# Performance work log

Hardware: AMD Instinct MI355X
Metric: run time of the kernel (lower is better)

Reference implementation:

```python
import jax, jax.numpy as jnp
import numpy as np

B, S, D = 2, 2048, 4096
H, KV, HD = 32, 8, 128          # n_heads, n_kv_heads, head_dim
N_REP = H // KV                  # GQA repeat factor = 4
ROPE_THETA = 500000.0


def _rope_tables(seqlen, head_dim, theta):
    inv_freq = 1.0 / (theta ** (np.arange(0, head_dim, 2, dtype=np.float32) / head_dim))
    angles = np.outer(np.arange(seqlen, dtype=np.float32), inv_freq)  # [S, HD/2]
    return jnp.asarray(np.cos(angles)), jnp.asarray(np.sin(angles))


def setup_inputs() -> dict:
    key = jax.random.key(0)
    ks = jax.random.split(key, 6)
    x = jax.random.normal(ks[0], (B, S, D), dtype=jnp.float32)
    freqs_cos, freqs_sin = _rope_tables(S, HD, ROPE_THETA)
    # causal additive mask, broadcast over (batch, heads)
    mask = jnp.where(jnp.tril(jnp.ones((S, S), dtype=bool)), 0.0, -jnp.inf).astype(jnp.float32)
    sc = 0.02
    wq = sc * jax.random.normal(ks[1], (D, H * HD), dtype=jnp.float32)   # (in, out)
    wk = sc * jax.random.normal(ks[2], (D, KV * HD), dtype=jnp.float32)
    wv = sc * jax.random.normal(ks[3], (D, KV * HD), dtype=jnp.float32)
    wo = sc * jax.random.normal(ks[4], (H * HD, D), dtype=jnp.float32)
    return {"x": x, "freqs_cos": freqs_cos, "freqs_sin": freqs_sin, "mask": mask,
            "wq": wq, "wk": wk, "wv": wv, "wo": wo}


def _apply_rope(t, cos, sin):
    # t: [B, S, nh, HD]; cos/sin: [S, HD/2]. Complex rotation on adjacent pairs.
    t2 = t.reshape(*t.shape[:-1], HD // 2, 2)
    t0, t1 = t2[..., 0], t2[..., 1]
    c = cos[None, :, None, :]
    s = sin[None, :, None, :]
    r0 = t0 * c - t1 * s
    r1 = t0 * s + t1 * c
    return jnp.stack([r0, r1], axis=-1).reshape(t.shape)


def reference(x, freqs_cos, freqs_sin, mask, wq, wk, wv, wo):
    bsz, seqlen, _ = x.shape
    xq = (x @ wq).reshape(bsz, seqlen, H, HD)
    xk = (x @ wk).reshape(bsz, seqlen, KV, HD)
    xv = (x @ wv).reshape(bsz, seqlen, KV, HD)
    xq = _apply_rope(xq, freqs_cos, freqs_sin)
    xk = _apply_rope(xk, freqs_cos, freqs_sin)
    # repeat_kv (GQA) -> [B, S, H, HD]
    keys = jnp.repeat(xk, N_REP, axis=2)
    values = jnp.repeat(xv, N_REP, axis=2)
    scores = jnp.einsum('bqhd,bkhd->bhqk', xq, keys) / jnp.sqrt(jnp.float32(HD))
    scores = scores + mask[None, None, :, :]
    probs = jax.nn.softmax(scores.astype(jnp.float32), axis=-1).astype(xq.dtype)
    out = jnp.einsum('bhqk,bkhd->bqhd', probs, values).reshape(bsz, seqlen, H * HD)
    return out @ wo
```

## Files before the change

kernel.cpp:

```cpp
#include <hip/hip_runtime.h>
#include <stdint.h>

#define B_ 2
#define S_ 2048
#define D_ 4096
#define H_ 32
#define KV_ 8
#define HD_ 128
#define M_ (B_*S_)
#define NQ_ (H_*HD_)
#define NKV_ (KV_*HD_)

typedef unsigned short u16;
typedef __bf16 bf16x8 __attribute__((ext_vector_type(8)));
typedef float f32x4 __attribute__((ext_vector_type(4)));
typedef u16 u16x8 __attribute__((ext_vector_type(8)));
typedef u16 u16x4 __attribute__((ext_vector_type(4)));

__device__ __forceinline__ u16 f2bf(float f) {
  union { float f; unsigned u; } v; v.f = f;
  unsigned r = v.u + 0x7fffu + ((v.u >> 16) & 1u);
  return (u16)(r >> 16);
}
__device__ __forceinline__ u16 f2bft(float f) {
  union { float f; unsigned u; } v; v.f = f;
  return (u16)(v.u >> 16);
}
__device__ __forceinline__ float bf2f(u16 u) {
  union { unsigned u; float f; } v; v.u = ((unsigned)u) << 16;
  return v.f;
}
__device__ __forceinline__ f32x4 mfma16(bf16x8 a, bf16x8 b, f32x4 c) {
  return __builtin_amdgcn_mfma_f32_16x16x32_bf16(a, b, c, 0, 0, 0);
}

#define GLDS16(gp, lp) __builtin_amdgcn_global_load_lds( \
    (const __attribute__((address_space(1))) unsigned int*)(gp), \
    (__attribute__((address_space(3))) unsigned int*)(lp), 16, 0, 0)

__global__ __launch_bounds__(256) void cvt_bf16(const float* __restrict__ in,
                                                u16* __restrict__ out, int n) {
  int i = (blockIdx.x * 256 + threadIdx.x) * 8;
  if (i >= n) return;
  float4 a = *(const float4*)(in + i);
  float4 b = *(const float4*)(in + i + 4);
  u16x8 o;
  o[0]=f2bf(a.x); o[1]=f2bf(a.y); o[2]=f2bf(a.z); o[3]=f2bf(a.w);
  o[4]=f2bf(b.x); o[5]=f2bf(b.y); o[6]=f2bf(b.z); o[7]=f2bf(b.w);
  *(u16x8*)(out + i) = o;
}

__global__ __launch_bounds__(256) void tcvt(const float* __restrict__ in,
                                            u16* __restrict__ out, int R, int C) {
  __shared__ __attribute__((aligned(16))) u16 tile[32][33];
  int c0 = blockIdx.x * 32, r0 = blockIdx.y * 32;
  int tx = threadIdx.x & 31, ty = threadIdx.x >> 5;
  #pragma unroll
  for (int j = ty; j < 32; j += 8)
    tile[j][tx] = f2bf(in[(size_t)(r0 + j) * C + c0 + tx]);
  __syncthreads();
  #pragma unroll
  for (int j = ty; j < 32; j += 8)
    out[(size_t)(c0 + j) * R + r0 + tx] = tile[tx][j];
}

template<int OUTMODE>
__global__ __launch_bounds__(256) void gemm_bt(const u16* __restrict__ A,
    const u16* __restrict__ BT, void* __restrict__ Cv, void* __restrict__ Cv2,
    int M, int N, int K) {
  __shared__ __attribute__((aligned(16))) u16 As[128 * 32];
  __shared__ __attribute__((aligned(16))) u16 Bs[128 * 32];
  const int tid = threadIdx.x;
  const int bn0 = blockIdx.x * 128, bm0 = blockIdx.y * 128;
  const int w = tid >> 6, l = tid & 63, g = l >> 4, q = l & 15;
  const int wm = (w >> 1) * 64, wn = (w & 1) * 64;
  f32x4 acc[4][4] = {};
  for (int kt = 0; kt < K; kt += 32) {
    __syncthreads();
    #pragma unroll
    for (int p = 0; p < 2; ++p) {
      int c = tid + p * 256;
      int row = c >> 2, slot = c & 3;
      int srck = (slot ^ ((row >> 1) & 3)) << 3;
      GLDS16(A + (size_t)(bm0 + row) * K + kt + srck, As + c * 8);
      GLDS16(BT + (size_t)(bn0 + row) * K + kt + srck, Bs + c * 8);
    }
    __syncthreads();
    bf16x8 af[4], bfr[4];
    #pragma unroll
    for (int m = 0; m < 4; ++m) {
      int row = wm + m * 16 + q;
      af[m] = *(const bf16x8*)(As + row * 32 + ((g ^ ((row >> 1) & 3)) << 3));
    }
    #pragma unroll
    for (int n = 0; n < 4; ++n) {
      int row = wn + n * 16 + q;
      bfr[n] = *(const bf16x8*)(Bs + row * 32 + ((g ^ ((row >> 1) & 3)) << 3));
    }
    #pragma unroll
    for (int m = 0; m < 4; ++m)
      #pragma unroll
      for (int n = 0; n < 4; ++n)
        acc[m][n] = mfma16(af[m], bfr[n], acc[m][n]);
  }
  #pragma unroll
  for (int m = 0; m < 4; ++m)
    #pragma unroll
    for (int n = 0; n < 4; ++n) {
      if (OUTMODE == 3) {
        int row0 = bm0 + wm + m * 16 + g * 4;
        int col  = bn0 + wn + n * 16 + q;
        if (col < 1024) {
          #pragma unroll
          for (int j = 0; j < 4; ++j)
            ((u16*)Cv)[(size_t)(row0 + j) * 1024 + col] = f2bf(acc[m][n][j]);
        } else {
          int c2 = col - 1024;
          u16x4 pk;
          #pragma unroll
          for (int j = 0; j < 4; ++j) pk[j] = f2bf(acc[m][n][j]);
          size_t off = ((size_t)((row0 >> 11) * KV_ + (c2 >> 7)) * 32 + ((row0 >> 6) & 31)) * 8192
                     + (size_t)(c2 & 127) * 64 + (row0 & 63);
          *(u16x4*)((u16*)Cv2 + off) = pk;
        }
      } else {
        #pragma unroll
        for (int j = 0; j < 4; ++j) {
          size_t off = (size_t)(bm0 + wm + m * 16 + g * 4 + j) * N + (bn0 + wn + n * 16 + q);
          if (OUTMODE == 1) ((float*)Cv)[off] = acc[m][n][j];
          else              ((u16*)Cv)[off]  = f2bf(acc[m][n][j]);
        }
      }
    }
}

template<int OUTMODE>
__global__ __launch_bounds__(512, 2) void gemm256(const u16* __restrict__ A,
    const u16* __restrict__ BT, void* __restrict__ Cv, int M, int N, int K) {
  extern __shared__ __attribute__((aligned(16))) u16 DL[];
  const int tid = threadIdx.x;
  const int bn0 = blockIdx.x * 256, bm0 = blockIdx.y * 256;
  const int l = tid & 63, g = l >> 4, q = l & 15;
  const int w = tid >> 6;
  const int wm = (w >> 2) * 128, wn = (w & 3) * 64;
  const int nt = K >> 6;
  f32x4 acc[8][4] = {};

  auto STAGE = [&](int t, int buf) {
    const int kt = t << 6;
    u16* Ad = DL + buf * 32768;
    u16* Bd = Ad + 16384;
    #pragma unroll
    for (int p = 0; p < 4; ++p) {
      int idx = tid + p * 512;
      int row = idx >> 3, slot = idx & 7;
      int sk = (slot ^ (row & 7)) << 3;
      GLDS16(A + (size_t)(bm0 + row) * K + kt + sk, Ad + idx * 8);
    }
    #pragma unroll
    for (int p = 0; p < 4; ++p) {
      int idx = tid + p * 512;
      int row = idx >> 3, slot = idx & 7;
      int sk = (slot ^ (row & 7)) << 3;
      GLDS16(BT + (size_t)(bn0 + row) * K + kt + sk, Bd + idx * 8);
    }
  };

  STAGE(0, 0);
  STAGE(1, 1);
  asm volatile("s_waitcnt vmcnt(8)" ::: "memory");
  __builtin_amdgcn_s_barrier();

  for (int t = 0; t < nt; ++t) {
    const int buf = t & 1;
    const u16* As = DL + buf * 32768;
    const u16* Bs = As + 16384;
    #pragma unroll
    for (int ks = 0; ks < 2; ++ks) {
      bf16x8 a[8], bb[2];
      #pragma unroll
      for (int m = 0; m < 8; ++m) {
        int row = wm + m * 16 + q;
        a[m] = *(const bf16x8*)(As + row * 64 + (((ks * 4 + g) ^ (row & 7)) << 3));
      }
      #pragma unroll
      for (int n = 0; n < 2; ++n) {
        int row = wn + n * 16 + q;
        bb[n] = *(const bf16x8*)(Bs + row * 64 + (((ks * 4 + g) ^ (row & 7)) << 3));
      }
      __builtin_amdgcn_s_setprio(1);
      #pragma unroll
      for (int m = 0; m < 8; ++m)
        #pragma unroll
        for (int n = 0; n < 2; ++n)
          acc[m][n] = mfma16(a[m], bb[n], acc[m][n]);
      __builtin_amdgcn_s_setprio(0);
      #pragma unroll
      for (int n = 0; n < 2; ++n) {
        int row = wn + (n + 2) * 16 + q;
        bb[n] = *(const bf16x8*)(Bs + row * 64 + (((ks * 4 + g) ^ (row & 7)) << 3));
      }
      __builtin_amdgcn_s_setprio(1);
      #pragma unroll
      for (int m = 0; m < 8; ++m)
        #pragma unroll
        for (int n = 0; n < 2; ++n)
          acc[m][n + 2] = mfma16(a[m], bb[n], acc[m][n + 2]);
      __builtin_amdgcn_s_setprio(0);
    }
    if (t + 1 < nt) {
      asm volatile("s_waitcnt lgkmcnt(0)" ::: "memory");
      __builtin_amdgcn_s_barrier();
      if (t + 2 < nt) {
        STAGE(t + 2, buf);
        asm volatile("s_waitcnt vmcnt(8)" ::: "memory");
      } else {
        asm volatile("s_waitcnt vmcnt(0)" ::: "memory");
      }
      __builtin_amdgcn_s_barrier();
    }
  }

  #pragma unroll
  for (int m = 0; m < 8; ++m)
    #pragma unroll
    for (int n = 0; n < 4; ++n)
      #pragma unroll
      for (int j = 0; j < 4; ++j) {
        size_t off = (size_t)(bm0 + wm + m * 16 + g * 4 + j) * N + (bn0 + wn + n * 16 + q);
        if (OUTMODE == 1) ((float*)Cv)[off] = acc[m][n][j];
        else              ((u16*)Cv)[off]  = f2bf(acc[m][n][j]);
      }
}

__global__ __launch_bounds__(256) void rope_kernel(u16* __restrict__ t,
    const float* __restrict__ fc, const float* __restrict__ fs,
    int log2ppr, int total_pairs) {
  int i = blockIdx.x * 256 + threadIdx.x;
  if (i >= total_pairs) return;
  int fi = i & 63;
  int row = i >> log2ppr;
  int pos = row & (S_ - 1);
  float c = fc[pos * 64 + fi], s = fs[pos * 64 + fi];
  unsigned* p = (unsigned*)(t + 2 * (size_t)i);
  unsigned v = *p;
  float x0 = bf2f((u16)(v & 0xffffu)), x1 = bf2f((u16)(v >> 16));
  float r0 = x0 * c - x1 * s, r1 = x0 * s + x1 * c;
  *p = (unsigned)f2bf(r0) | ((unsigned)f2bf(r1) << 16);
}

__global__ __launch_bounds__(256, 4) void attn_kernel(
    const u16* __restrict__ Qb, const u16* __restrict__ Kb,
    const u16* __restrict__ VTg, u16* __restrict__ Ob) {
  __shared__ __attribute__((aligned(16))) u16 SM[20480];
  u16* Ks = SM;
  u16* Vs = SM + 8192;
  u16* Ps = SM + 16384;
  const int pr = blockIdx.x;
  const int h = blockIdx.y, b = blockIdx.z;
  const int kvh = h >> 2;
  const int tid = threadIdx.x, w = tid >> 6, l = tid & 63, g = l >> 4, ql = l & 15;
  const float SL2E = 0.08838834764831845f * 1.4426950408889634f;
  const u16* Qh = Qb + (size_t)b * S_ * NQ_ + h * HD_;
  const u16* Kh = Kb + ((size_t)b * S_ * KV_ + kvh) * HD_;
  const u16* Vh = VTg + (size_t)(b * KV_ + kvh) * (32 * 8192);
  u16* Oh = Ob + (size_t)b * S_ * NQ_ + h * HD_;

  for (int ph = 0; ph < 2; ++ph) {
    const int qt = ph ? pr : 31 - pr;
    __syncthreads();
    bf16x8 aq[4];
    #pragma unroll
    for (int kk = 0; kk < 4; ++kk)
      aq[kk] = *(const bf16x8*)(Qh + (size_t)(qt * 64 + w * 16 + ql) * NQ_ + kk * 32 + g * 8);

    f32x4 o[8] = {};
    float mrow = -3.0e38f, lrow = 0.f;

    const int nkt = qt + 1;
    for (int kt = 0; kt < nkt; ++kt) {
      #pragma unroll
      for (int p = 0; p < 4; ++p) {
        int c = tid + p * 256;
        int row = c >> 4, slot = c & 15;
        GLDS16(Kh + (size_t)(kt * 64 + row) * (KV_ * HD_) + ((slot ^ (row & 7)) << 3), Ks + c * 8);
      }
      #pragma unroll
      for (int p = 0; p < 4; ++p) {
        int c = tid + p * 256;
        int row = c >> 3, slot = c & 7;
        GLDS16(Vh + (size_t)kt * 8192 + row * 64 + ((slot ^ (row & 7)) << 3), Vs + c * 8);
      }
      asm volatile("s_waitcnt vmcnt(0)" ::: "memory");
      __builtin_amdgcn_s_barrier();

      if (kt * 64 <= qt * 64 + w * 16 + 15) {
        f32x4 sc[4] = {};
        #pragma unroll
        for (int kk = 0; kk < 4; ++kk) {
          bf16x8 bk[4];
          #pragma unroll
          for (int n = 0; n < 4; ++n) {
            int row = n * 16 + ql;
            bk[n] = *(const bf16x8*)(Ks + row * 128 + (((kk * 4 + g) ^ (row & 7)) << 3));
          }
          #pragma unroll
          for (int n = 0; n < 4; ++n)
            sc[n] = mfma16(bk[n], aq[kk], sc[n]);
        }
        const int qglob = qt * 64 + w * 16 + ql;
        if (kt * 64 + 63 > qt * 64 + w * 16) {
          #pragma unroll
          for (int n = 0; n < 4; ++n)
            #pragma unroll
            for (int j = 0; j < 4; ++j)
              if (kt * 64 + n * 16 + g * 4 + j > qglob) sc[n][j] = -3.0e38f;
        }
        float mx = sc[0][0];
        #pragma unroll
        for (int n = 0; n < 4; ++n)
          #pragma unroll
          for (int j = 0; j < 4; ++j) mx = fmaxf(mx, sc[n][j]);
        mx = fmaxf(mx, __shfl_xor(mx, 16));
        mx = fmaxf(mx, __shfl_xor(mx, 32));
        if (!__all(mx - mrow <= 16.0f)) {
          float mnew = fmaxf(mrow, mx);
          float f = exp2f((mrow - mnew) * SL2E);
          lrow *= f;
          #pragma unroll
          for (int m = 0; m < 8; ++m) o[m] *= f;
          mrow = mnew;
        }
        float rs = 0.f;
        #pragma unroll
        for (int n = 0; n < 4; ++n)
          #pragma unroll
          for (int j = 0; j < 4; ++j) {
            float pv = exp2f((sc[n][j] - mrow) * SL2E);
            sc[n][j] = pv; rs += pv;
          }
        rs += __shfl_xor(rs, 16);
        rs += __shfl_xor(rs, 32);
        lrow += rs;
        u16* Pw = Ps + w * 1024;
        #pragma unroll
        for (int n = 0; n < 4; ++n) {
          u16x4 pk;
          #pragma unroll
          for (int j = 0; j < 4; ++j) pk[j] = f2bft(sc[n][j]);
          *(u16x4*)(Pw + ql * 64 + (((n * 2 + (g >> 1)) ^ (ql & 7)) << 3) + (g & 1) * 4) = pk;
        }
        #pragma unroll
        for (int kk2 = 0; kk2 < 2; ++kk2) {
          bf16x8 bp = *(const bf16x8*)(Pw + ql * 64 + (((kk2 * 4 + g) ^ (ql & 7)) << 3));
          #pragma unroll
          for (int m = 0; m < 8; ++m) {
            int row = m * 16 + ql;
            bf16x8 av = *(const bf16x8*)(Vs + row * 64 + (((kk2 * 4 + g) ^ (row & 7)) << 3));
            o[m] = mfma16(av, bp, o[m]);
          }
        }
      }
      __builtin_amdgcn_s_barrier();
    }
    __syncthreads();
    u16* OS = SM;
    float linv = 1.0f / lrow;
    #pragma unroll
    for (int m = 0; m < 8; ++m)
      #pragma unroll
      for (int j = 0; j < 4; ++j)
        OS[(w * 16 + ql) * 136 + m * 16 + g * 4 + j] = f2bf(o[m][j] * linv);
    __syncthreads();
    #pragma unroll
    for (int p = 0; p < 4; ++p) {
      int c = tid + p * 256;
      int row = c >> 4, col8 = c & 15;
      u16x8 d = *(const u16x8*)(OS + row * 136 + col8 * 8);
      *(u16x8*)(Oh + (size_t)(qt * 64 + row) * NQ_ + col8 * 8) = d;
    }
  }
}

extern "C" void kernel_launch(void* const* d_in, const int* in_sizes, int n_in,
                              void* d_out, int out_size, void* d_ws, size_t ws_size,
                              hipStream_t stream) {
  const float* x  = (const float*)d_in[0];
  const float* fc = (const float*)d_in[1];
  const float* fs = (const float*)d_in[2];
  const float* wq = (const float*)d_in[4];
  const float* wk = (const float*)d_in[5];
  const float* wv = (const float*)d_in[6];
  const float* wo = (const float*)d_in[7];

  char* ws = (char*)d_ws;
  u16* xb  = (u16*)(ws + 0);
  u16* wqT = (u16*)(ws + 33554432);
  u16* wkT = (u16*)(ws + 67108864);
  u16* wvT = (u16*)(ws + 75497472);
  u16* woT = (u16*)(ws + 83886080);
  u16* qb  = (u16*)(ws + 117440512);
  u16* kb  = (u16*)(ws + 150994944);
  u16* vtg = (u16*)(ws + 159383552);
  u16* ob  = (u16*)(ws + 167772160);
  if (ws_size < 201326592u) return;

  cvt_bf16<<<(M_ * D_) / (8 * 256), 256, 0, stream>>>(x, xb, M_ * D_);
  tcvt<<<dim3(NQ_ / 32, D_ / 32), 256, 0, stream>>>(wq, wqT, D_, NQ_);
  tcvt<<<dim3(NKV_ / 32, D_ / 32), 256, 0, stream>>>(wk, wkT, D_, NKV_);
  tcvt<<<dim3(NKV_ / 32, D_ / 32), 256, 0, stream>>>(wv, wvT, D_, NKV_);
  tcvt<<<dim3(D_ / 32, NQ_ / 32), 256, 0, stream>>>(wo, woT, NQ_, D_);

  gemm256<0><<<dim3(NQ_ / 256, M_ / 256), 512, 131072, stream>>>(xb, wqT, qb, M_, NQ_, D_);
  gemm_bt<3><<<dim3(2048 / 128, M_ / 128), 256, 0, stream>>>(xb, wkT, kb, vtg, M_, 2048, D_);

  rope_kernel<<<(M_ * NQ_ / 2) / 256, 256, 0, stream>>>(qb, fc, fs, 11, M_ * NQ_ / 2);
  rope_kernel<<<(M_ * NKV_ / 2) / 256, 256, 0, stream>>>(kb, fc, fs, 9, M_ * NKV_ / 2);

  attn_kernel<<<dim3(16, H_, B_), 256, 0, stream>>>(qb, kb, vtg, ob);

  gemm256<1><<<dim3(D_ / 256, M_ / 256), 512, 131072, stream>>>(ob, woT, d_out, M_, D_, NQ_);
}
```

Measured before the change: 587.7 us.

## Add XCD-aware block remap and four-phase barrier-synchronized schedule to gemm256

The 2D grid becomes a 1D grid, and block IDs are remapped so that consecutive tiles land on the same XCD (8 chiplets), with the aim of better L2 reuse. The K-tile inner loop is split into four phases, each loading A/B fragments from LDS and then running MFMAs between s_barriers with sched_barrier fences, so warps interleave LDS reads and MFMA work in lockstep. The A prefetch is issued earlier, in the last phase, and the B prefetch comes afterward. The added barriers may increase synchronization stalls, and correctness depends on the swizzle mapping staying bijective for these grid sizes.

```diff
diff --git a/kernel.cpp b/kernel.cpp
--- a/kernel.cpp
+++ b/kernel.cpp
@@ -139,35 +139,39 @@
     const u16* __restrict__ BT, void* __restrict__ Cv, int M, int N, int K) {
   extern __shared__ __attribute__((aligned(16))) u16 DL[];
   const int tid = threadIdx.x;
-  const int bn0 = blockIdx.x * 256, bm0 = blockIdx.y * 256;
+  const int nbx = N >> 8;
+  const int cpx = gridDim.x >> 3;
+  const int swzb = (blockIdx.x & 7) * cpx + (blockIdx.x >> 3);
+  const int bn0 = (swzb % nbx) << 8, bm0 = (swzb / nbx) << 8;
   const int l = tid & 63, g = l >> 4, q = l & 15;
   const int w = tid >> 6;
   const int wm = (w >> 2) * 128, wn = (w & 3) * 64;
   const int nt = K >> 6;
   f32x4 acc[8][4] = {};
 
-  auto STAGE = [&](int t, int buf) {
+  auto STAGE_A = [&](int t, int buf) {
     const int kt = t << 6;
     u16* Ad = DL + buf * 32768;
-    u16* Bd = Ad + 16384;
     #pragma unroll
     for (int p = 0; p < 4; ++p) {
       int idx = tid + p * 512;
       int row = idx >> 3, slot = idx & 7;
-      int sk = (slot ^ (row & 7)) << 3;
-      GLDS16(A + (size_t)(bm0 + row) * K + kt + sk, Ad + idx * 8);
-    }
+      GLDS16(A + (size_t)(bm0 + row) * K + kt + ((slot ^ (row & 7)) << 3), Ad + idx * 8);
+    }
+  };
+  auto STAGE_B = [&](int t, int buf) {
+    const int kt = t << 6;
+    u16* Bd = DL + buf * 32768 + 16384;
     #pragma unroll
     for (int p = 0; p < 4; ++p) {
       int idx = tid + p * 512;
       int row = idx >> 3, slot = idx & 7;
-      int sk = (slot ^ (row & 7)) << 3;
-      GLDS16(BT + (size_t)(bn0 + row) * K + kt + sk, Bd + idx * 8);
+      GLDS16(BT + (size_t)(bn0 + row) * K + kt + ((slot ^ (row & 7)) << 3), Bd + idx * 8);
     }
   };
 
-  STAGE(0, 0);
-  STAGE(1, 1);
+  STAGE_A(0, 0); STAGE_B(0, 0);
+  STAGE_A(1, 1); STAGE_B(1, 1);
   asm volatile("s_waitcnt vmcnt(8)" ::: "memory");
   __builtin_amdgcn_s_barrier();
 
@@ -175,44 +179,86 @@
     const int buf = t & 1;
     const u16* As = DL + buf * 32768;
     const u16* Bs = As + 16384;
-    #pragma unroll
-    for (int ks = 0; ks < 2; ++ks) {
-      bf16x8 a[8], bb[2];
+    bf16x8 a[8];
+
+    {
+      bf16x8 b0, b1;
       #pragma unroll
       for (int m = 0; m < 8; ++m) {
         int row = wm + m * 16 + q;
-        a[m] = *(const bf16x8*)(As + row * 64 + (((ks * 4 + g) ^ (row & 7)) << 3));
-      }
-      #pragma unroll
-      for (int n = 0; n < 2; ++n) {
-        int row = wn + n * 16 + q;
-        bb[n] = *(const bf16x8*)(Bs + row * 64 + (((ks * 4 + g) ^ (row & 7)) << 3));
-      }
+        a[m] = *(const bf16x8*)(As + row * 64 + ((g ^ (row & 7)) << 3));
+      }
+      { int row = wn + q;      b0 = *(const bf16x8*)(Bs + row * 64 + ((g ^ (row & 7)) << 3)); }
+      { int row = wn + 16 + q; b1 = *(const bf16x8*)(Bs + row * 64 + ((g ^ (row & 7)) << 3)); }
+      __builtin_amdgcn_s_barrier();
+      asm volatile("s_waitcnt lgkmcnt(0)" ::: "memory");
+      __builtin_amdgcn_sched_barrier(0);
       __builtin_amdgcn_s_setprio(1);
       #pragma unroll
-      for (int m = 0; m < 8; ++m)
-        #pragma unroll
-        for (int n = 0; n < 2; ++n)
-          acc[m][n] = mfma16(a[m], bb[n], acc[m][n]);
+      for (int m = 0; m < 8; ++m) {
+        acc[m][0] = mfma16(a[m], b0, acc[m][0]);
+        acc[m][1] = mfma16(a[m], b1, acc[m][1]);
+      }
       __builtin_amdgcn_s_setprio(0);
-      #pragma unroll
-      for (int n = 0; n < 2; ++n) {
-        int row = wn + (n + 2) * 16 + q;
-        bb[n] = *(const bf16x8*)(Bs + row * 64 + (((ks * 4 + g) ^ (row & 7)) << 3));
-      }
+      __builtin_amdgcn_s_barrier();
+    }
+    {
+      bf16x8 b2, b3;
+      { int row = wn + 32 + q; b2 = *(const bf16x8*)(Bs + row * 64 + ((g ^ (row & 7)) << 3)); }
+      { int row = wn + 48 + q; b3 = *(const bf16x8*)(Bs + row * 64 + ((g ^ (row & 7)) << 3)); }
+      __builtin_amdgcn_s_barrier();
+      asm volatile("s_waitcnt lgkmcnt(0)" ::: "memory");
+      __builtin_amdgcn_sched_barrier(0);
       __builtin_amdgcn_s_setprio(1);
       #pragma unroll
-      for (int m = 0; m < 8; ++m)
-        #pragma unroll
-        for (int n = 0; n < 2; ++n)
-          acc[m][n + 2] = mfma16(a[m], bb[n], acc[m][n + 2]);
+      for (int m = 0; m < 8; ++m) {
+        acc[m][2] = mfma16(a[m], b2, acc[m][2]);
+        acc[m][3] = mfma16(a[m], b3, acc[m][3]);
+      }
       __builtin_amdgcn_s_setprio(0);
+      __builtin_amdgcn_s_barrier();
+    }
+    {
+      bf16x8 b0, b1;
+      #pragma unroll
+      for (int m = 0; m < 8; ++m) {
+        int row = wm + m * 16 + q;
+        a[m] = *(const bf16x8*)(As + row * 64 + (((4 + g) ^ (row & 7)) << 3));
+      }
+      { int row = wn + q;      b0 = *(const bf16x8*)(Bs + row * 64 + (((4 + g) ^ (row & 7)) << 3)); }
+      { int row = wn + 16 + q; b1 = *(const bf16x8*)(Bs + row * 64 + (((4 + g) ^ (row & 7)) << 3)); }
+      __builtin_amdgcn_s_barrier();
+      asm volatile("s_waitcnt lgkmcnt(0)" ::: "memory");
+      __builtin_amdgcn_sched_barrier(0);
+      __builtin_amdgcn_s_setprio(1);
+      #pragma unroll
+      for (int m = 0; m < 8; ++m) {
+        acc[m][0] = mfma16(a[m], b0, acc[m][0]);
+        acc[m][1] = mfma16(a[m], b1, acc[m][1]);
+      }
+      __builtin_amdgcn_s_setprio(0);
+      __builtin_amdgcn_s_barrier();
+    }
+    {
+      if (t + 2 < nt) STAGE_A(t + 2, buf);
+      bf16x8 b2, b3;
+      { int row = wn + 32 + q; b2 = *(const bf16x8*)(Bs + row * 64 + (((4 + g) ^ (row & 7)) << 3)); }
+      { int row = wn + 48 + q; b3 = *(const bf16x8*)(Bs + row * 64 + (((4 + g) ^ (row & 7)) << 3)); }
+      __builtin_amdgcn_s_barrier();
+      asm volatile("s_waitcnt lgkmcnt(0)" ::: "memory");
+      __builtin_amdgcn_sched_barrier(0);
+      __builtin_amdgcn_s_setprio(1);
+      #pragma unroll
+      for (int m = 0; m < 8; ++m) {
+        acc[m][2] = mfma16(a[m], b2, acc[m][2]);
+        acc[m][3] = mfma16(a[m], b3, acc[m][3]);
+      }
+      __builtin_amdgcn_s_setprio(0);
+      __builtin_amdgcn_s_barrier();
     }
     if (t + 1 < nt) {
-      asm volatile("s_waitcnt lgkmcnt(0)" ::: "memory");
-      __builtin_amdgcn_s_barrier();
       if (t + 2 < nt) {
-        STAGE(t + 2, buf);
+        STAGE_B(t + 2, buf);
         asm volatile("s_waitcnt vmcnt(8)" ::: "memory");
       } else {
         asm volatile("s_waitcnt vmcnt(0)" ::: "memory");
@@ -411,7 +457,7 @@
   tcvt<<<dim3(NKV_ / 32, D_ / 32), 256, 0, stream>>>(wv, wvT, D_, NKV_);
   tcvt<<<dim3(D_ / 32, NQ_ / 32), 256, 0, stream>>>(wo, woT, NQ_, D_);
 
-  gemm256<0><<<dim3(NQ_ / 256, M_ / 256), 512, 131072, stream>>>(xb, wqT, qb, M_, NQ_, D_);
+  gemm256<0><<<(NQ_ / 256) * (M_ / 256), 512, 131072, stream>>>(xb, wqT, qb, M_, NQ_, D_);
   gemm_bt<3><<<dim3(2048 / 128, M_ / 128), 256, 0, stream>>>(xb, wkT, kb, vtg, M_, 2048, D_);
 
   rope_kernel<<<(M_ * NQ_ / 2) / 256, 256, 0, stream>>>(qb, fc, fs, 11, M_ * NQ_ / 2);
@@ -419,5 +465,5 @@
 
   attn_kernel<<<dim3(16, H_, B_), 256, 0, stream>>>(qb, kb, vtg, ob);
 
-  gemm256<1><<<dim3(D_ / 256, M_ / 256), 512, 131072, stream>>>(ob, woT, d_out, M_, D_, NQ_);
-}
+  gemm256<1><<<(D_ / 256) * (M_ / 256), 512, 131072, stream>>>(ob, woT, d_out, M_, D_, NQ_);
+}
```

Measured after the change: 583.9 us. No clear change (-0.6%).

## Restructure gemm256 into 3-stage BK=32 pipeline with register double-buffered A and XCD swizzle

Applied to the files above, without the earlier changes.

Rewrites the 256x256 GEMM mainloop to use a K-tile of 32 with a three-buffer LDS ring (96 KB instead of 128 KB), a single barrier per tile, and A fragments prefetched into registers for the next tile while MFMAs run on the current one. Blocks are launched as a 1D grid and remapped with an XCD-aware swizzle so neighbouring tiles share L2 on the same die. The aim is to reduce barrier/LDS stalls and improve cache locality for the Q and output projections. The cost is more barriers per unit of K, and the extra A registers may add register pressure.

```diff
diff --git a/kernel.cpp b/kernel.cpp
--- a/kernel.cpp
+++ b/kernel.cpp
@@ -139,86 +139,73 @@
     const u16* __restrict__ BT, void* __restrict__ Cv, int M, int N, int K) {
   extern __shared__ __attribute__((aligned(16))) u16 DL[];
   const int tid = threadIdx.x;
-  const int bn0 = blockIdx.x * 256, bm0 = blockIdx.y * 256;
+  const int nbx = N >> 8;
+  const int cpx = gridDim.x >> 3;
+  const int swzb = (blockIdx.x & 7) * cpx + (blockIdx.x >> 3);
+  const int bn0 = (swzb % nbx) << 8, bm0 = (swzb / nbx) << 8;
   const int l = tid & 63, g = l >> 4, q = l & 15;
   const int w = tid >> 6;
   const int wm = (w >> 2) * 128, wn = (w & 3) * 64;
-  const int nt = K >> 6;
+  const int nt = K >> 5;
   f32x4 acc[8][4] = {};
 
-  auto STAGE = [&](int t, int buf) {
-    const int kt = t << 6;
-    u16* Ad = DL + buf * 32768;
-    u16* Bd = Ad + 16384;
-    #pragma unroll
-    for (int p = 0; p < 4; ++p) {
-      int idx = tid + p * 512;
-      int row = idx >> 3, slot = idx & 7;
-      int sk = (slot ^ (row & 7)) << 3;
-      GLDS16(A + (size_t)(bm0 + row) * K + kt + sk, Ad + idx * 8);
-    }
-    #pragma unroll
-    for (int p = 0; p < 4; ++p) {
-      int idx = tid + p * 512;
-      int row = idx >> 3, slot = idx & 7;
-      int sk = (slot ^ (row & 7)) << 3;
-      GLDS16(BT + (size_t)(bn0 + row) * K + kt + sk, Bd + idx * 8);
-    }
+  const int srow = tid >> 2, schunk = tid & 3;
+  const int ssw = (schunk ^ ((srow >> 1) & 3)) << 3;
+  const u16* gA0 = A  + (size_t)(bm0 + srow) * K + ssw;
+  const u16* gA1 = gA0 + (size_t)128 * K;
+  const u16* gB0 = BT + (size_t)(bn0 + srow) * K + ssw;
+  const u16* gB1 = gB0 + (size_t)128 * K;
+
+  auto STAGE = [&](int t) {
+    const int kt = t << 5;
+    u16* d = DL + (t % 3) * 16384;
+    GLDS16(gA0 + kt, d + tid * 8);
+    GLDS16(gA1 + kt, d + 4096 + tid * 8);
+    GLDS16(gB0 + kt, d + 8192 + tid * 8);
+    GLDS16(gB1 + kt, d + 12288 + tid * 8);
   };
 
-  STAGE(0, 0);
-  STAGE(1, 1);
-  asm volatile("s_waitcnt vmcnt(8)" ::: "memory");
+  const u16* ra = DL + (wm + q) * 32 + ((g ^ (((wm + q) >> 1) & 3)) << 3);
+  const u16* rb = DL + 8192 + (wn + q) * 32 + ((g ^ (((wn + q) >> 1) & 3)) << 3);
+
+  bf16x8 aC[8], aN[8];
+
+  STAGE(0); STAGE(1);
+  asm volatile("s_waitcnt vmcnt(4)" ::: "memory");
   __builtin_amdgcn_s_barrier();
-
-  for (int t = 0; t < nt; ++t) {
-    const int buf = t & 1;
-    const u16* As = DL + buf * 32768;
-    const u16* Bs = As + 16384;
-    #pragma unroll
-    for (int ks = 0; ks < 2; ++ks) {
-      bf16x8 a[8], bb[2];
-      #pragma unroll
-      for (int m = 0; m < 8; ++m) {
-        int row = wm + m * 16 + q;
-        a[m] = *(const bf16x8*)(As + row * 64 + (((ks * 4 + g) ^ (row & 7)) << 3));
-      }
-      #pragma unroll
-      for (int n = 0; n < 2; ++n) {
-        int row = wn + n * 16 + q;
-        bb[n] = *(const bf16x8*)(Bs + row * 64 + (((ks * 4 + g) ^ (row & 7)) << 3));
-      }
-      __builtin_amdgcn_s_setprio(1);
-      #pragma unroll
-      for (int m = 0; m < 8; ++m)
-        #pragma unroll
-        for (int n = 0; n < 2; ++n)
-          acc[m][n] = mfma16(a[m], bb[n], acc[m][n]);
-      __builtin_amdgcn_s_setprio(0);
-      #pragma unroll
-      for (int n = 0; n < 2; ++n) {
-        int row = wn + (n + 2) * 16 + q;
-        bb[n] = *(const bf16x8*)(Bs + row * 64 + (((ks * 4 + g) ^ (row & 7)) << 3));
-      }
-      __builtin_amdgcn_s_setprio(1);
-      #pragma unroll
-      for (int m = 0; m < 8; ++m)
-        #pragma unroll
-        for (int n = 0; n < 2; ++n)
-          acc[m][n + 2] = mfma16(a[m], bb[n], acc[m][n + 2]);
-      __builtin_amdgcn_s_setprio(0);
-    }
+  #pragma unroll
+  for (int m = 0; m < 8; ++m) aC[m] = *(const bf16x8*)(ra + m * 512);
+
+  auto TILE = [&](int t, bf16x8 (&ac)[8], bf16x8 (&an)[8]) {
+    if (t + 2 < nt) {
+      STAGE(t + 2);
+      asm volatile("s_waitcnt vmcnt(4)" ::: "memory");
+    } else {
+      asm volatile("s_waitcnt vmcnt(0)" ::: "memory");
+    }
+    __builtin_amdgcn_s_barrier();
+    const u16* pb = rb + (t % 3) * 16384;
+    bf16x8 b0 = *(const bf16x8*)(pb);
+    bf16x8 b1 = *(const bf16x8*)(pb + 512);
+    bf16x8 b2 = *(const bf16x8*)(pb + 1024);
+    bf16x8 b3 = *(const bf16x8*)(pb + 1536);
     if (t + 1 < nt) {
-      asm volatile("s_waitcnt lgkmcnt(0)" ::: "memory");
-      __builtin_amdgcn_s_barrier();
-      if (t + 2 < nt) {
-        STAGE(t + 2, buf);
-        asm volatile("s_waitcnt vmcnt(8)" ::: "memory");
-      } else {
-        asm volatile("s_waitcnt vmcnt(0)" ::: "memory");
-      }
-      __builtin_amdgcn_s_barrier();
-    }
+      const u16* pa = ra + ((t + 1) % 3) * 16384;
+      #pragma unroll
+      for (int m = 0; m < 8; ++m) an[m] = *(const bf16x8*)(pa + m * 512);
+    }
+    #pragma unroll
+    for (int m = 0; m < 8; ++m) {
+      acc[m][0] = mfma16(ac[m], b0, acc[m][0]);
+      acc[m][1] = mfma16(ac[m], b1, acc[m][1]);
+      acc[m][2] = mfma16(ac[m], b2, acc[m][2]);
+      acc[m][3] = mfma16(ac[m], b3, acc[m][3]);
+    }
+  };
+
+  for (int t = 0; t < nt; t += 2) {
+    TILE(t,     aC, aN);
+    TILE(t + 1, aN, aC);
   }
 
   #pragma unroll
@@ -411,7 +398,7 @@
   tcvt<<<dim3(NKV_ / 32, D_ / 32), 256, 0, stream>>>(wv, wvT, D_, NKV_);
   tcvt<<<dim3(D_ / 32, NQ_ / 32), 256, 0, stream>>>(wo, woT, NQ_, D_);
 
-  gemm256<0><<<dim3(NQ_ / 256, M_ / 256), 512, 131072, stream>>>(xb, wqT, qb, M_, NQ_, D_);
+  gemm256<0><<<(NQ_ / 256) * (M_ / 256), 512, 98304, stream>>>(xb, wqT, qb, M_, NQ_, D_);
   gemm_bt<3><<<dim3(2048 / 128, M_ / 128), 256, 0, stream>>>(xb, wkT, kb, vtg, M_, 2048, D_);
 
   rope_kernel<<<(M_ * NQ_ / 2) / 256, 256, 0, stream>>>(qb, fc, fs, 11, M_ * NQ_ / 2);
@@ -419,5 +406,5 @@
 
   attn_kernel<<<dim3(16, H_, B_), 256, 0, stream>>>(qb, kb, vtg, ob);
 
-  gemm256<1><<<dim3(D_ / 256, M_ / 256), 512, 131072, stream>>>(ob, woT, d_out, M_, D_, NQ_);
-}
+  gemm256<1><<<(D_ / 256) * (M_ / 256), 512, 98304, stream>>>(ob, woT, d_out, M_, D_, NQ_);
+}
```

Result: no change. 581.0 us (-1.1%).
